# Optimization experiments

Measured on AMD Instinct MI355X. Metric: run time of the kernel, lower is better.

The kernel has to match this reference:

```python
import jax, jax.numpy as jnp
import numpy as np

V, E, H = 32000, 512, 1024
B, TS, TP = 32, 50, 32


def build_sparse_u_input(slot_np):
    # faithful jnp version of get_sparse_selective_input (vocab.decode EOS check skipped)
    ts, b = slot_np.shape
    res = jnp.full((ts, b, V + ts), 1e-10, dtype=jnp.float32)
    copy_mask = (slot_np == 2) | (slot_np >= V)
    add_mask = (slot_np != 0) & (~copy_mask)
    ti = jnp.arange(ts)[:, None]
    bi = jnp.arange(b)[None, :]
    res = res.at[ti, bi, slot_np].add(add_mask.astype(jnp.float32))
    res = res.at[ti, bi, V + ti].add((5.0 - 1e-10) * copy_mask.astype(jnp.float32))
    return jnp.transpose(res, (1, 0, 2))  # [B, Ts, V+Ts]


def setup_inputs() -> dict:
    key = jax.random.key(0)
    ks = jax.random.split(key, 20)
    s = lambda d: 1.0 / np.sqrt(d)
    slot_np = jax.random.randint(ks[0], (TS, B), 0, V)
    inp = {
        'slot_enc_out': jax.random.normal(ks[1], (TS, B, H), jnp.float32),
        'personality_enc_out': jax.random.normal(ks[2], (TP, B, H), jnp.float32),
        'last_hidden': jax.random.normal(ks[3], (1, B, H), jnp.float32),
        'm_t_input': jax.random.randint(ks[4], (1, B), 0, V),
        'slot_np': slot_np,
        'sparse_u_input': build_sparse_u_input(slot_np),
        'emb': jax.random.normal(ks[5], (V, E), jnp.float32),
        'W_attn_a': jax.random.normal(ks[6], (H, 2 * H), jnp.float32) * s(2 * H),
        'b_attn_a': jnp.zeros((H,), jnp.float32),
        'v_a': jax.random.normal(ks[7], (H,), jnp.float32) * s(H),
        'W_attn_p': jax.random.normal(ks[8], (H, 2 * H), jnp.float32) * s(2 * H),
        'b_attn_p': jnp.zeros((H,), jnp.float32),
        'v_p': jax.random.normal(ks[9], (H,), jnp.float32) * s(H),
        'W_ih': jax.random.normal(ks[10], (3 * H, E + 2 * H), jnp.float32) * s(E + 2 * H),
        'W_hh': jax.random.normal(ks[11], (3 * H, H), jnp.float32) * s(H),
        'b_ih': jnp.zeros((3 * H,), jnp.float32),
        'b_hh': jnp.zeros((3 * H,), jnp.float32),
        'W_proj': jax.random.normal(ks[12], (V, 3 * H), jnp.float32) * s(3 * H),
        'b_proj': jnp.zeros((V,), jnp.float32),
        'W_c2': jax.random.normal(ks[13], (H, H), jnp.float32) * s(H),
        'b_c2': jnp.zeros((H,), jnp.float32),
    }
    return inp


def _attn(hidden, enc, W, b, v):
    # hidden: [1,B,H], enc: [T,B,H] -> context [B,H]
    enc_b = jnp.swapaxes(enc, 0, 1)                       # [B,T,H]
    Hh = jnp.broadcast_to(hidden[0][:, None, :], enc_b.shape)
    e = jnp.tanh(jnp.concatenate([Hh, enc_b], -1) @ W.T + b)  # [B,T,H]
    a = jax.nn.softmax(jnp.einsum('bth,h->bt', e, v), axis=-1)
    return jnp.einsum('bt,bth->bh', a, enc_b)


def _gru_cell(x, h, W_ih, W_hh, b_ih, b_hh):
    gi = x @ W_ih.T + b_ih
    gh = h @ W_hh.T + b_hh
    ir, iz, inn = jnp.split(gi, 3, axis=-1)
    hr, hz, hn = jnp.split(gh, 3, axis=-1)
    r = jax.nn.sigmoid(ir + hr)
    z = jax.nn.sigmoid(iz + hz)
    n = jnp.tanh(inn + r * hn)
    return (1.0 - z) * n + z * h


def reference(slot_enc_out, personality_enc_out, last_hidden, m_t_input, slot_np,
              sparse_u_input, emb, W_attn_a, b_attn_a, v_a, W_attn_p, b_attn_p, v_p,
              W_ih, W_hh, b_ih, b_hh, W_proj, b_proj, W_c2, b_c2):
    m_embed = emb[m_t_input[0]]                                    # [B,E]
    a_ctx = _attn(last_hidden, slot_enc_out, W_attn_a, b_attn_a, v_a)
    p_ctx = _attn(last_hidden, personality_enc_out, W_attn_p, b_attn_p, v_p)
    gru_in = jnp.concatenate([m_embed, a_ctx, p_ctx], axis=-1)     # [B,E+2H]
    h_new = _gru_cell(gru_in, last_hidden[0], W_ih, W_hh, b_ih, b_hh)  # [B,H]
    gen_score = jnp.concatenate([a_ctx, p_ctx, h_new], -1) @ W_proj.T + b_proj  # [B,V]
    # copy score
    uc = jnp.tanh(jnp.swapaxes(slot_enc_out, 0, 1) @ W_c2.T + b_c2)  # [B,Ts,H]
    u = jnp.einsum('bth,bh->bt', uc, h_new)                          # [B,Ts]
    m = jnp.max(u, axis=1, keepdims=True)
    u = jnp.exp(u - m)
    u = jnp.log(jnp.einsum('bt,btv->bv', u, sparse_u_input)) + m     # [B,V+Ts]
    scores = jax.nn.softmax(jnp.concatenate([gen_score, u], axis=1), axis=1)
    gen, cp = scores[:, :V], scores[:, V:]
    proba = jnp.concatenate([gen + cp[:, :V], cp[:, V:]], axis=1)    # [B,V+Ts]
    return proba, h_new[None], h_new[None]
```

## Files before the change

### kernel.cpp

```cpp
#include <hip/hip_runtime.h>
#include <math.h>

static constexpr int V_   = 32000;
static constexpr int E_   = 512;
static constexpr int H_   = 1024;
static constexpr int B_   = 32;
static constexpr int TS_  = 50;
static constexpr int TP_  = 32;
static constexpr int VTS  = V_ + TS_;
static constexpr int H3   = 3 * H_;
static constexpr int GIN_ = E_ + 2 * H_;
static constexpr int NS   = 8;
static constexpr int SLE  = (VTS + NS - 1) / NS;
static constexpr int GSL  = V_ / NS;
static constexpr int PSK  = 12;

__global__ void zero_gather(float* __restrict__ extra,
                            const float* __restrict__ emb,
                            const int* __restrict__ mt,
                            float* __restrict__ gx)
{
    const int i = blockIdx.x * 256 + threadIdx.x;
    if (i < B_ * VTS) extra[i] = 0.f;
    if (i < B_ * E_) gx[i] = emb[(size_t)mt[i >> 9] * E_ + (i & 511)];
}

__device__ __forceinline__ void m32v2_tile(
    const float* __restrict__ A, int lda,
    const float* __restrict__ W, int ldw, int wko,
    int klen, int n0, float* __restrict__ po, int N)
{
    __shared__ float As[32][36];
    __shared__ float Ws[32][257];

    const int tid  = threadIdx.x;
    const int lane = tid & 63;
    const int wv   = tid >> 6;
    const int wq   = lane & 7;
    const int wg   = lane >> 3;
    const int am   = tid >> 3;
    const int aq   = tid & 7;

    float acc[8][4];
#pragma unroll
    for (int i = 0; i < 8; ++i)
#pragma unroll
        for (int j = 0; j < 4; ++j) acc[i][j] = 0.f;

    float4 a4 = *reinterpret_cast<const float4*>(A + (size_t)am * lda + 4 * aq);
    float4 w4[8];
#pragma unroll
    for (int i = 0; i < 8; ++i)
        w4[i] = *reinterpret_cast<const float4*>(
            W + (size_t)(n0 + wv * 64 + i * 8 + wg) * ldw + wko + 4 * wq);

    for (int kb = 0; kb < klen; kb += 32) {
        __syncthreads();
        As[4 * aq + 0][am] = a4.x; As[4 * aq + 1][am] = a4.y;
        As[4 * aq + 2][am] = a4.z; As[4 * aq + 3][am] = a4.w;
#pragma unroll
        for (int i = 0; i < 8; ++i) {
            const int col = wv * 64 + i * 8 + wg;
            Ws[4 * wq + 0][col] = w4[i].x; Ws[4 * wq + 1][col] = w4[i].y;
            Ws[4 * wq + 2][col] = w4[i].z; Ws[4 * wq + 3][col] = w4[i].w;
        }
        __syncthreads();
        if (kb + 32 < klen) {
            a4 = *reinterpret_cast<const float4*>(A + (size_t)am * lda + kb + 32 + 4 * aq);
#pragma unroll
            for (int i = 0; i < 8; ++i)
                w4[i] = *reinterpret_cast<const float4*>(
                    W + (size_t)(n0 + wv * 64 + i * 8 + wg) * ldw + wko + kb + 32 + 4 * wq);
        }
#pragma unroll 8
        for (int k = 0; k < 32; ++k) {
            const float4 a0 = *reinterpret_cast<const float4*>(&As[k][wv * 8]);
            const float4 a1 = *reinterpret_cast<const float4*>(&As[k][wv * 8 + 4]);
            const float av[8] = {a0.x, a0.y, a0.z, a0.w, a1.x, a1.y, a1.z, a1.w};
            const float w0 = Ws[k][lane];
            const float w1 = Ws[k][lane + 64];
            const float w2 = Ws[k][lane + 128];
            const float w3 = Ws[k][lane + 192];
#pragma unroll
            for (int i = 0; i < 8; ++i) {
                acc[i][0] = fmaf(av[i], w0, acc[i][0]);
                acc[i][1] = fmaf(av[i], w1, acc[i][1]);
                acc[i][2] = fmaf(av[i], w2, acc[i][2]);
                acc[i][3] = fmaf(av[i], w3, acc[i][3]);
            }
        }
    }
#pragma unroll
    for (int i = 0; i < 8; ++i) {
        float* op = po + (size_t)(wv * 8 + i) * N + n0;
#pragma unroll
        for (int j = 0; j < 4; ++j)
            op[lane + 64 * j] = acc[i][j];
    }
}

__global__ __launch_bounds__(256)
void gemm_hid(const float* __restrict__ hid,
              const float* __restrict__ Wa, const float* __restrict__ Wp,
              float* __restrict__ parts)
{
    const int z = blockIdx.z, y = blockIdx.y, n0 = blockIdx.x * 256;
    const float* W = z ? Wp : Wa;
    m32v2_tile(hid + y * 256, H_, W, 2 * H_, y * 256, 256, n0,
               parts + (size_t)(z * 4 + y) * B_ * H_, H_);
}

__global__ __launch_bounds__(256)
void gemm_gru(const float* __restrict__ gx, const float* __restrict__ ctxa,
              const float* __restrict__ ctxp, const float* __restrict__ hid,
              const float* __restrict__ W_ih, const float* __restrict__ W_hh,
              float* __restrict__ parts)
{
    const int y = blockIdx.y, n0 = blockIdx.x * 256;
    const float* A; int lda; const float* W; int ldw; int wko; int klo;
    if (y < 2)       { klo = y * 256;        A = gx;   lda = E_; W = W_ih; ldw = GIN_; wko = klo; }
    else if (y < 6)  { klo = (y - 2) * 256;  A = ctxa; lda = H_; W = W_ih; ldw = GIN_; wko = 512 + klo; }
    else if (y < 10) { klo = (y - 6) * 256;  A = ctxp; lda = H_; W = W_ih; ldw = GIN_; wko = 1536 + klo; }
    else             { klo = (y - 10) * 256; A = hid;  lda = H_; W = W_hh; ldw = H_;   wko = klo; }
    m32v2_tile(A + klo, lda, W, ldw, wko, 256, n0,
               parts + (size_t)y * B_ * H3, H3);
}

__global__ void reduce_gru(const float* __restrict__ parts,
                           const float* __restrict__ b_ih, const float* __restrict__ b_hh,
                           const float* __restrict__ hid,
                           float* __restrict__ hnew,
                           float* __restrict__ o2, float* __restrict__ o3)
{
    const int i = blockIdx.x * 256 + threadIdx.x;
    if (i >= B_ * H_) return;
    const int b = i >> 10, j = i & 1023;
    float gi[3], gh[3];
#pragma unroll
    for (int c = 0; c < 3; ++c) {
        float s = b_ih[c * H_ + j];
        for (int y = 0; y < 10; ++y)
            s += parts[((size_t)y * B_ + b) * H3 + c * H_ + j];
        gi[c] = s;
        float t = b_hh[c * H_ + j];
        for (int y = 10; y < 14; ++y)
            t += parts[((size_t)y * B_ + b) * H3 + c * H_ + j];
        gh[c] = t;
    }
    const float r = 1.f / (1.f + expf(-(gi[0] + gh[0])));
    const float z = 1.f / (1.f + expf(-(gi[1] + gh[1])));
    const float n = tanhf(gi[2] + r * gh[2]);
    const float o = (1.f - z) * n + z * hid[i];
    hnew[i] = o; o2[i] = o; o3[i] = o;
}

__global__ __launch_bounds__(256)
void gemm_proj(const float* __restrict__ ctxa, const float* __restrict__ ctxp,
               const float* __restrict__ hnew, const float* __restrict__ W_proj,
               float* __restrict__ parts)
{
    const int y = blockIdx.y, n0 = blockIdx.x * 256;
    const int slice = y >> 2, kq = y & 3;
    const float* A = (slice == 0) ? ctxa : (slice == 1) ? ctxp : hnew;
    m32v2_tile(A + kq * 256, H_, W_proj, H3, slice * 1024 + kq * 256,
               256, n0, parts + (size_t)y * B_ * V_, V_);
}

__global__ __launch_bounds__(256)
void gemm_tall84(const float* __restrict__ slot_enc, const float* __restrict__ pers_enc,
                 const float* __restrict__ W_attn_a, const float* __restrict__ W_attn_p,
                 const float* __restrict__ W_c2,
                 const float* __restrict__ b_attn_a, const float* __restrict__ b_attn_p,
                 const float* __restrict__ b_c2,
                 const float* __restrict__ v_a, const float* __restrict__ v_p,
                 const float* __restrict__ parts,
                 float* __restrict__ SA, float* __restrict__ SP, float* __restrict__ UCt)
{
    __shared__ float As[32][68];
    __shared__ float Ws[32][132];
    const int z = blockIdx.z;
    const float* A; const float* W; float* C; int M, ldw;
    if (z == 0)      { A = slot_enc; W = W_attn_a + H_; C = SA;  M = TS_ * B_; ldw = 2 * H_; }
    else if (z == 1) { A = pers_enc; W = W_attn_p + H_; C = SP;  M = TP_ * B_; ldw = 2 * H_; }
    else             { A = slot_enc; W = W_c2;          C = UCt; M = TS_ * B_; ldw = H_; }
    const int m0 = blockIdx.x * 64;
    if (m0 >= M) return;
    const int n0 = blockIdx.y * 128;
    const int tid = threadIdx.x;
    const int tym = tid >> 5;
    const int txn = tid & 31;
    const int sr = tid & 63, sh = tid >> 6;
    const int wr = tid & 127, wh = tid >> 7;

    float acc[8][4];
#pragma unroll
    for (int i = 0; i < 8; ++i)
#pragma unroll
        for (int j = 0; j < 4; ++j) acc[i][j] = 0.f;

    float4 a4[2], w4[4];
#pragma unroll
    for (int q = 0; q < 2; ++q)
        a4[q] = *reinterpret_cast<const float4*>(A + (size_t)(m0 + sr) * H_ + 8 * sh + 4 * q);
#pragma unroll
    for (int q = 0; q < 4; ++q)
        w4[q] = *reinterpret_cast<const float4*>(W + (size_t)(n0 + wr) * ldw + 16 * wh + 4 * q);

    for (int kb = 0; kb < H_; kb += 32) {
        __syncthreads();
#pragma unroll
        for (int q = 0; q < 2; ++q) {
            As[8 * sh + 4 * q + 0][sr] = a4[q].x; As[8 * sh + 4 * q + 1][sr] = a4[q].y;
            As[8 * sh + 4 * q + 2][sr] = a4[q].z; As[8 * sh + 4 * q + 3][sr] = a4[q].w;
        }
#pragma unroll
        for (int q = 0; q < 4; ++q) {
            Ws[16 * wh + 4 * q + 0][wr] = w4[q].x; Ws[16 * wh + 4 * q + 1][wr] = w4[q].y;
            Ws[16 * wh + 4 * q + 2][wr] = w4[q].z; Ws[16 * wh + 4 * q + 3][wr] = w4[q].w;
        }
        __syncthreads();
        if (kb + 32 < H_) {
#pragma unroll
            for (int q = 0; q < 2; ++q)
                a4[q] = *reinterpret_cast<const float4*>(A + (size_t)(m0 + sr) * H_ + kb + 32 + 8 * sh + 4 * q);
#pragma unroll
            for (int q = 0; q < 4; ++q)
                w4[q] = *reinterpret_cast<const float4*>(W + (size_t)(n0 + wr) * ldw + kb + 32 + 16 * wh + 4 * q);
        }
#pragma unroll 8
        for (int k = 0; k < 32; ++k) {
            const float4 a0 = *reinterpret_cast<const float4*>(&As[k][8 * tym]);
            const float4 a1 = *reinterpret_cast<const float4*>(&As[k][8 * tym + 4]);
            const float av[8] = {a0.x, a0.y, a0.z, a0.w, a1.x, a1.y, a1.z, a1.w};
            const float w0 = Ws[k][txn];
            const float w1 = Ws[k][txn + 32];
            const float w2 = Ws[k][txn + 64];
            const float w3 = Ws[k][txn + 96];
#pragma unroll
            for (int i = 0; i < 8; ++i) {
                acc[i][0] = fmaf(av[i], w0, acc[i][0]);
                acc[i][1] = fmaf(av[i], w1, acc[i][1]);
                acc[i][2] = fmaf(av[i], w2, acc[i][2]);
                acc[i][3] = fmaf(av[i], w3, acc[i][3]);
            }
        }
    }

    if (z < 2) {
        const float* bvec = z ? b_attn_p : b_attn_a;
        const float* vvec = z ? v_p : v_a;
        const float* pp = parts + (size_t)(z * 4) * B_ * H_;
#pragma unroll
        for (int i = 0; i < 8; ++i) {
            const int row = m0 + 8 * tym + i;
            const int b = row & 31;
#pragma unroll
            for (int j = 0; j < 4; ++j) {
                const int col = n0 + txn + 32 * j;
                float ha = bvec[col];
#pragma unroll
                for (int ss = 0; ss < 4; ++ss)
                    ha += pp[((size_t)ss * B_ + b) * H_ + col];
                C[(size_t)row * H_ + col] = tanhf(acc[i][j] + ha) * vvec[col];
            }
        }
    } else {
#pragma unroll
        for (int i = 0; i < 8; ++i) {
            const int row = m0 + 8 * tym + i;
#pragma unroll
            for (int j = 0; j < 4; ++j) {
                const int col = n0 + txn + 32 * j;
                C[(size_t)row * H_ + col] = tanhf(acc[i][j] + b_c2[col]);
            }
        }
    }
}

__global__ __launch_bounds__(512)
void attn_fused2(const float* __restrict__ SA, const float* __restrict__ SP,
                 const float* __restrict__ slot_enc, const float* __restrict__ pers_enc,
                 float* __restrict__ ctxa, float* __restrict__ ctxp)
{
    const int b = blockIdx.x, z = blockIdx.y;
    const int T = z ? TP_ : TS_;
    const float* S   = z ? SP : SA;
    const float* enc = z ? pers_enc : slot_enc;
    float* ctx       = z ? ctxp : ctxa;

    const int tid  = threadIdx.x;
    const int wave = tid >> 6;
    const int lane = tid & 63;
    __shared__ float sc[64];
    __shared__ float aw[64];

    for (int t = wave; t < T; t += 8) {
        const float* e = S + ((size_t)t * B_ + b) * H_;
        float p = 0.f;
        for (int j = lane; j < H_; j += 64) p += e[j];
#pragma unroll
        for (int off = 32; off > 0; off >>= 1) p += __shfl_down(p, off);
        if (lane == 0) sc[t] = p;
    }
    __syncthreads();
    if (tid < 64) {
        const float x = (tid < T) ? sc[tid] : -3.4e38f;
        float mx = x;
#pragma unroll
        for (int off = 32; off > 0; off >>= 1) mx = fmaxf(mx, __shfl_xor(mx, off));
        const float ex = (tid < T) ? expf(x - mx) : 0.f;
        float sm = ex;
#pragma unroll
        for (int off = 32; off > 0; off >>= 1) sm += __shfl_xor(sm, off);
        aw[tid] = ex / sm;
    }
    __syncthreads();
    for (int k = tid; k < H_; k += 512) {
        float c = 0.f;
        for (int t = 0; t < T; ++t)
            c += aw[t] * enc[((size_t)t * B_ + b) * H_ + k];
        ctx[(size_t)b * H_ + k] = c;
    }
}

__global__ __launch_bounds__(512)
void u_prep_scatter2(const float* __restrict__ UCt, const float* __restrict__ hn,
                     const int* __restrict__ slot_np,
                     float* __restrict__ mS, float* __restrict__ extra)
{
    const int b    = blockIdx.x;
    const int tid  = threadIdx.x;
    const int wave = tid >> 6;
    const int lane = tid & 63;
    __shared__ float su[64];
    __shared__ float eu_s[64];

    const float* h = hn + (size_t)b * H_;
    for (int t = wave; t < TS_; t += 8) {
        const float* r = UCt + ((size_t)t * B_ + b) * H_;
        float p = 0.f;
        for (int j = lane; j < H_; j += 64)
            p += r[j] * h[j];
#pragma unroll
        for (int off = 32; off > 0; off >>= 1) p += __shfl_down(p, off);
        if (lane == 0) su[t] = p;
    }
    __syncthreads();
    if (tid < 64) {
        const float x = (tid < TS_) ? su[tid] : -3.4e38f;
        float mx = x;
#pragma unroll
        for (int off = 32; off > 0; off >>= 1) mx = fmaxf(mx, __shfl_xor(mx, off));
        const float ex = (tid < TS_) ? expf(x - mx) : 0.f;
        float sm = ex;
#pragma unroll
        for (int off = 32; off > 0; off >>= 1) sm += __shfl_xor(sm, off);
        eu_s[tid] = ex;
        if (tid == 0) { mS[b * 2] = mx; mS[b * 2 + 1] = sm; }
    }
    __syncthreads();
    if (tid < TS_) {
        const int sv = slot_np[tid * B_ + b];
        const float e = eu_s[tid];
        const bool copy = (sv == 2) || (sv >= V_);
        const bool add  = (sv != 0) && !copy;
        if (add)  atomicAdd(&extra[(size_t)b * VTS + sv], e);
        if (copy) atomicAdd(&extra[(size_t)b * VTS + V_ + tid], 5.0f * e);
    }
}

__device__ __forceinline__ float blk_reduce(float v, float* red, int tid, bool ismax)
{
    red[tid] = v; __syncthreads();
    for (int s = 128; s > 0; s >>= 1) {
        if (tid < s) red[tid] = ismax ? fmaxf(red[tid], red[tid + s]) : (red[tid] + red[tid + s]);
        __syncthreads();
    }
    const float r = red[0]; __syncthreads();
    return r;
}

__global__ __launch_bounds__(256)
void ph_max2g(const float* __restrict__ parts, const float* __restrict__ b_proj,
              const float* __restrict__ extra,
              float* __restrict__ gen,
              float* __restrict__ pgm, float* __restrict__ pzs,
              float* __restrict__ pem, float* __restrict__ pes)
{
    const int b = blockIdx.x, s = blockIdx.y, tid = threadIdx.x;
    __shared__ float red[256];
    const int g0 = s * GSL;

    float gv[16];
    float gm = -3.4e38f;
#pragma unroll
    for (int u = 0; u < 16; ++u) {
        const int loc = tid + 256 * u;
        float val = -3.4e38f;
        if (loc < GSL) {
            const int idx = g0 + loc;
            float ssum = 0.f;
#pragma unroll
            for (int ss = 0; ss < PSK; ++ss)
                ssum += parts[((size_t)ss * B_ + b) * V_ + idx];
            val = ssum + b_proj[idx];
            gen[(size_t)b * V_ + idx] = val;
            gm = fmaxf(gm, val);
        }
        gv[u] = val;
    }
    gm = blk_reduce(gm, red, tid, true);
    float zs = 0.f;
#pragma unroll
    for (int u = 0; u < 16; ++u)
        zs += expf(gv[u] - gm);
    zs = blk_reduce(zs, red, tid, false);

    const float* ex = extra + (size_t)b * VTS;
    const int e0 = s * SLE;
    const int e1 = (e0 + SLE < VTS) ? e0 + SLE : VTS;
    float em = 0.f, es = 0.f;
    for (int i = e0 + tid; i < e1; i += 256) { const float v = ex[i]; em = fmaxf(em, v); es += v; }
    em = blk_reduce(em, red, tid, true);
    es = blk_reduce(es, red, tid, false);
    if (tid == 0) {
        pgm[b * NS + s] = gm; pzs[b * NS + s] = zs;
        pem[b * NS + s] = em; pes[b * NS + s] = es;
    }
}

__global__ __launch_bounds__(256)
void ph_write2(const float* __restrict__ gen, const float* __restrict__ extra,
               const float* __restrict__ pgm, const float* __restrict__ pzs,
               const float* __restrict__ pem, const float* __restrict__ pes,
               const float* __restrict__ mS, float* __restrict__ proba)
{
    const int b = blockIdx.x, s = blockIdx.y, tid = threadIdx.x;
    const float mb   = mS[b * 2];
    const float Sb   = mS[b * 2 + 1];
    const float base = 1e-10f * Sb;

    float gm = -3.4e38f, em = 0.f;
#pragma unroll
    for (int k = 0; k < NS; ++k) {
        gm = fmaxf(gm, pgm[b * NS + k]);
        em = fmaxf(em, pem[b * NS + k]);
    }
    const float M = fmaxf(gm, mb + logf(base + em));
    float s1 = 0.f, s2 = 0.f;
#pragma unroll
    for (int k = 0; k < NS; ++k) {
        s1 += pzs[b * NS + k] * expf(pgm[b * NS + k] - M);
        s2 += pes[b * NS + k];
    }
    const float cs  = expf(mb - M);
    const float inv = 1.f / (s1 + cs * (base * VTS + s2));

    const float* g  = gen + (size_t)b * V_;
    const float* ex = extra + (size_t)b * VTS;
    float* o = proba + (size_t)b * VTS;
    const int e0 = s * SLE;
    const int e1 = (e0 + SLE < VTS) ? e0 + SLE : VTS;
    for (int i = e0 + tid; i < e1; i += 256) {
        const float cp = cs * (base + ex[i]) * inv;
        o[i] = (i < V_) ? (expf(g[i] - M) * inv + cp) : cp;
    }
}

extern "C" void kernel_launch(void* const* d_in, const int* in_sizes, int n_in,
                              void* d_out, int out_size, void* d_ws, size_t ws_size,
                              hipStream_t stream)
{
    const float* slot_enc = (const float*)d_in[0];
    const float* pers_enc = (const float*)d_in[1];
    const float* hid      = (const float*)d_in[2];
    const int*   mt       = (const int*)d_in[3];
    const int*   slot_np  = (const int*)d_in[4];
    const float* emb      = (const float*)d_in[6];
    const float* W_attn_a = (const float*)d_in[7];
    const float* b_attn_a = (const float*)d_in[8];
    const float* v_a      = (const float*)d_in[9];
    const float* W_attn_p = (const float*)d_in[10];
    const float* b_attn_p = (const float*)d_in[11];
    const float* v_p      = (const float*)d_in[12];
    const float* W_ih     = (const float*)d_in[13];
    const float* W_hh     = (const float*)d_in[14];
    const float* b_ih     = (const float*)d_in[15];
    const float* b_hh     = (const float*)d_in[16];
    const float* W_proj   = (const float*)d_in[17];
    const float* b_proj   = (const float*)d_in[18];
    const float* W_c2     = (const float*)d_in[19];
    const float* b_c2     = (const float*)d_in[20];
    float* out = (float*)d_out;

    float* w = (float*)d_ws;
    size_t off = 0;
    auto alloc = [&](size_t n) { float* p = w + off; off += n; return p; };
    float* SA    = alloc((size_t)TS_ * B_ * H_);
    float* SP    = alloc((size_t)TP_ * B_ * H_);
    float* UCt   = alloc((size_t)TS_ * B_ * H_);
    float* ctxa  = alloc((size_t)B_ * H_);
    float* ctxp  = alloc((size_t)B_ * H_);
    float* gx    = alloc((size_t)B_ * E_);
    float* hnew  = alloc((size_t)B_ * H_);
    float* gen   = alloc((size_t)B_ * V_);
    float* mS    = alloc((size_t)2 * B_);
    float* extra = alloc((size_t)B_ * VTS);
    float* pgm   = alloc((size_t)B_ * NS);
    float* pzs   = alloc((size_t)B_ * NS);
    float* pem   = alloc((size_t)B_ * NS);
    float* pes   = alloc((size_t)B_ * NS);
    float* parts = w + off;

    const int o2 = B_ * VTS;
    const int o3 = o2 + B_ * H_;

    zero_gather<<<(B_ * VTS + 255) / 256, 256, 0, stream>>>(extra, emb, mt, gx);

    gemm_hid<<<dim3(4, 4, 2), 256, 0, stream>>>(hid, W_attn_a, W_attn_p, parts);

    gemm_tall84<<<dim3(25, 8, 3), 256, 0, stream>>>(
        slot_enc, pers_enc, W_attn_a, W_attn_p, W_c2,
        b_attn_a, b_attn_p, b_c2, v_a, v_p, parts, SA, SP, UCt);

    attn_fused2<<<dim3(B_, 2), 512, 0, stream>>>(SA, SP, slot_enc, pers_enc, ctxa, ctxp);

    gemm_gru<<<dim3(12, 14), 256, 0, stream>>>(gx, ctxa, ctxp, hid, W_ih, W_hh, parts);
    reduce_gru<<<(B_ * H_ + 255) / 256, 256, 0, stream>>>(parts, b_ih, b_hh, hid, hnew, out + o2, out + o3);

    gemm_proj<<<dim3(125, PSK), 256, 0, stream>>>(ctxa, ctxp, hnew, W_proj, parts);

    u_prep_scatter2<<<B_, 512, 0, stream>>>(UCt, hnew, slot_np, mS, extra);

    ph_max2g<<<dim3(B_, NS), 256, 0, stream>>>(parts, b_proj, extra, gen, pgm, pzs, pem, pes);
    ph_write2<<<dim3(B_, NS), 256, 0, stream>>>(gen, extra, pgm, pzs, pem, pes, mS, out);
}
```

Measured before the change: 471.2 us.

## Merge ctx-part projection GEMM with GRU GEMM; defer h_new slice to separate launch

```diff
diff --git a/kernel.cpp b/kernel.cpp
--- a/kernel.cpp
+++ b/kernel.cpp
@@ -111,19 +111,39 @@
 }
 
 __global__ __launch_bounds__(256)
-void gemm_gru(const float* __restrict__ gx, const float* __restrict__ ctxa,
-              const float* __restrict__ ctxp, const float* __restrict__ hid,
+void gemm_pcg(const float* __restrict__ ctxa, const float* __restrict__ ctxp,
+              const float* __restrict__ hid, const float* __restrict__ gx,
+              const float* __restrict__ W_proj,
               const float* __restrict__ W_ih, const float* __restrict__ W_hh,
-              float* __restrict__ parts)
+              float* __restrict__ partsP, float* __restrict__ partsG)
+{
+    const int bid = blockIdx.x;
+    if (bid < 1000) {
+        const int y = bid / 125, n0 = (bid % 125) * 256;
+        const int slice = y >> 2, kq = y & 3;
+        const float* A = slice ? ctxp : ctxa;
+        m32v2_tile(A + kq * 256, H_, W_proj, H3, slice * 1024 + kq * 256,
+                   256, n0, partsP + (size_t)y * B_ * V_, V_);
+    } else {
+        const int idx = bid - 1000;
+        const int y = idx / 12, n0 = (idx % 12) * 256;
+        const float* A; int lda; const float* W; int ldw; int wko; int klo;
+        if (y < 2)       { klo = y * 256;        A = gx;   lda = E_; W = W_ih; ldw = GIN_; wko = klo; }
+        else if (y < 6)  { klo = (y - 2) * 256;  A = ctxa; lda = H_; W = W_ih; ldw = GIN_; wko = 512 + klo; }
+        else if (y < 10) { klo = (y - 6) * 256;  A = ctxp; lda = H_; W = W_ih; ldw = GIN_; wko = 1536 + klo; }
+        else             { klo = (y - 10) * 256; A = hid;  lda = H_; W = W_hh; ldw = H_;   wko = klo; }
+        m32v2_tile(A + klo, lda, W, ldw, wko, 256, n0,
+                   partsG + (size_t)y * B_ * H3, H3);
+    }
+}
+
+__global__ __launch_bounds__(256)
+void gemm_projh(const float* __restrict__ hnew, const float* __restrict__ W_proj,
+                float* __restrict__ partsP)
 {
     const int y = blockIdx.y, n0 = blockIdx.x * 256;
-    const float* A; int lda; const float* W; int ldw; int wko; int klo;
-    if (y < 2)       { klo = y * 256;        A = gx;   lda = E_; W = W_ih; ldw = GIN_; wko = klo; }
-    else if (y < 6)  { klo = (y - 2) * 256;  A = ctxa; lda = H_; W = W_ih; ldw = GIN_; wko = 512 + klo; }
-    else if (y < 10) { klo = (y - 6) * 256;  A = ctxp; lda = H_; W = W_ih; ldw = GIN_; wko = 1536 + klo; }
-    else             { klo = (y - 10) * 256; A = hid;  lda = H_; W = W_hh; ldw = H_;   wko = klo; }
-    m32v2_tile(A + klo, lda, W, ldw, wko, 256, n0,
-               parts + (size_t)y * B_ * H3, H3);
+    m32v2_tile(hnew + y * 256, H_, W_proj, H3, 2048 + y * 256,
+               256, n0, partsP + (size_t)(8 + y) * B_ * V_, V_);
 }
 
 __global__ void reduce_gru(const float* __restrict__ parts,
@@ -152,18 +172,6 @@
     const float n = tanhf(gi[2] + r * gh[2]);
     const float o = (1.f - z) * n + z * hid[i];
     hnew[i] = o; o2[i] = o; o3[i] = o;
-}
-
-__global__ __launch_bounds__(256)
-void gemm_proj(const float* __restrict__ ctxa, const float* __restrict__ ctxp,
-               const float* __restrict__ hnew, const float* __restrict__ W_proj,
-               float* __restrict__ parts)
-{
-    const int y = blockIdx.y, n0 = blockIdx.x * 256;
-    const int slice = y >> 2, kq = y & 3;
-    const float* A = (slice == 0) ? ctxa : (slice == 1) ? ctxp : hnew;
-    m32v2_tile(A + kq * 256, H_, W_proj, H3, slice * 1024 + kq * 256,
-               256, n0, parts + (size_t)y * B_ * V_, V_);
 }
 
 __global__ __launch_bounds__(256)
@@ -277,17 +285,11 @@
     }
 }
 
-__global__ __launch_bounds__(512)
-void attn_fused2(const float* __restrict__ SA, const float* __restrict__ SP,
-                 const float* __restrict__ slot_enc, const float* __restrict__ pers_enc,
-                 float* __restrict__ ctxa, float* __restrict__ ctxp)
-{
-    const int b = blockIdx.x, z = blockIdx.y;
-    const int T = z ? TP_ : TS_;
-    const float* S   = z ? SP : SA;
-    const float* enc = z ? pers_enc : slot_enc;
-    float* ctx       = z ? ctxp : ctxa;
-
+template <int T>
+__device__ __forceinline__ void attn_body(const float* __restrict__ S,
+                                          const float* __restrict__ enc,
+                                          float* __restrict__ ctx, int b)
+{
     const int tid  = threadIdx.x;
     const int wave = tid >> 6;
     const int lane = tid & 63;
@@ -297,7 +299,8 @@
     for (int t = wave; t < T; t += 8) {
         const float* e = S + ((size_t)t * B_ + b) * H_;
         float p = 0.f;
-        for (int j = lane; j < H_; j += 64) p += e[j];
+#pragma unroll
+        for (int j = 0; j < H_ / 64; ++j) p += e[lane + 64 * j];
 #pragma unroll
         for (int off = 32; off > 0; off >>= 1) p += __shfl_down(p, off);
         if (lane == 0) sc[t] = p;
@@ -317,10 +320,21 @@
     __syncthreads();
     for (int k = tid; k < H_; k += 512) {
         float c = 0.f;
+#pragma unroll 10
         for (int t = 0; t < T; ++t)
             c += aw[t] * enc[((size_t)t * B_ + b) * H_ + k];
         ctx[(size_t)b * H_ + k] = c;
     }
+}
+
+__global__ __launch_bounds__(512)
+void attn_fused3(const float* __restrict__ SA, const float* __restrict__ SP,
+                 const float* __restrict__ slot_enc, const float* __restrict__ pers_enc,
+                 float* __restrict__ ctxa, float* __restrict__ ctxp)
+{
+    const int b = blockIdx.x;
+    if (blockIdx.y == 0) attn_body<TS_>(SA, slot_enc, ctxa, b);
+    else                 attn_body<TP_>(SP, pers_enc, ctxp, b);
 }
 
 __global__ __launch_bounds__(512)
@@ -339,8 +353,9 @@
     for (int t = wave; t < TS_; t += 8) {
         const float* r = UCt + ((size_t)t * B_ + b) * H_;
         float p = 0.f;
-        for (int j = lane; j < H_; j += 64)
-            p += r[j] * h[j];
+#pragma unroll
+        for (int j = 0; j < H_ / 64; ++j)
+            p += r[lane + 64 * j] * h[lane + 64 * j];
 #pragma unroll
         for (int off = 32; off > 0; off >>= 1) p += __shfl_down(p, off);
         if (lane == 0) su[t] = p;
@@ -510,28 +525,33 @@
     float* pzs   = alloc((size_t)B_ * NS);
     float* pem   = alloc((size_t)B_ * NS);
     float* pes   = alloc((size_t)B_ * NS);
-    float* parts = w + off;
+    float* partsP = alloc((size_t)PSK * B_ * V_);
+    float* partsG = alloc((size_t)14 * B_ * H3);
+    float* partsH = partsG;
+    float* partsHd = alloc((size_t)8 * B_ * H_);
 
     const int o2 = B_ * VTS;
     const int o3 = o2 + B_ * H_;
+    (void)partsH;
 
     zero_gather<<<(B_ * VTS + 255) / 256, 256, 0, stream>>>(extra, emb, mt, gx);
 
-    gemm_hid<<<dim3(4, 4, 2), 256, 0, stream>>>(hid, W_attn_a, W_attn_p, parts);
+    gemm_hid<<<dim3(4, 4, 2), 256, 0, stream>>>(hid, W_attn_a, W_attn_p, partsHd);
 
     gemm_tall84<<<dim3(25, 8, 3), 256, 0, stream>>>(
         slot_enc, pers_enc, W_attn_a, W_attn_p, W_c2,
-        b_attn_a, b_attn_p, b_c2, v_a, v_p, parts, SA, SP, UCt);
-
-    attn_fused2<<<dim3(B_, 2), 512, 0, stream>>>(SA, SP, slot_enc, pers_enc, ctxa, ctxp);
-
-    gemm_gru<<<dim3(12, 14), 256, 0, stream>>>(gx, ctxa, ctxp, hid, W_ih, W_hh, parts);
-    reduce_gru<<<(B_ * H_ + 255) / 256, 256, 0, stream>>>(parts, b_ih, b_hh, hid, hnew, out + o2, out + o3);
-
-    gemm_proj<<<dim3(125, PSK), 256, 0, stream>>>(ctxa, ctxp, hnew, W_proj, parts);
+        b_attn_a, b_attn_p, b_c2, v_a, v_p, partsHd, SA, SP, UCt);
+
+    attn_fused3<<<dim3(B_, 2), 512, 0, stream>>>(SA, SP, slot_enc, pers_enc, ctxa, ctxp);
+
+    gemm_pcg<<<1168, 256, 0, stream>>>(ctxa, ctxp, hid, gx, W_proj, W_ih, W_hh, partsP, partsG);
+
+    reduce_gru<<<(B_ * H_ + 255) / 256, 256, 0, stream>>>(partsG, b_ih, b_hh, hid, hnew, out + o2, out + o3);
+
+    gemm_projh<<<dim3(125, 4), 256, 0, stream>>>(hnew, W_proj, partsP);
 
     u_prep_scatter2<<<B_, 512, 0, stream>>>(UCt, hnew, slot_np, mS, extra);
 
-    ph_max2g<<<dim3(B_, NS), 256, 0, stream>>>(parts, b_proj, extra, gen, pgm, pzs, pem, pes);
+    ph_max2g<<<dim3(B_, NS), 256, 0, stream>>>(partsP, b_proj, extra, gen, pgm, pzs, pem, pes);
     ph_write2<<<dim3(B_, NS), 256, 0, stream>>>(gen, extra, pgm, pzs, pem, pes, mS, out);
 }
```

Measured after the change: 403.7 us. -14.3%, faster.
